# Performance work log

Measured on AMD Instinct MI355X. Metric: run time of the kernel, lower is better.

## Reference

```python
import jax, jax.numpy as jnp
import numpy as np

# Bit-slice configuration from the module defaults: slices [1,1,2,4] -> 8-bit signed INT.
# The crossbar engine's MapReduceDot decomposes the quantized integers into bit-planes,
# runs partial dot products per (input-slice, weight-slice) pair across paral_size
# partitions, and recombines them with 2^shift weights. In the ideal (noise-free)
# engine this recombination is EXACT, so the forward math equals:
#   dequant(blockwise_quant(x)) @ dequant(blockwise_quant(W^T)) + bias
# with per-block scales determined by the quant granularities.
IN_BITS = 1 + 1 + 2 + 4   # sum(input_slice)  = 8
W_BITS = 1 + 1 + 2 + 4    # sum(weight_slice) = 8
IN_GRAN = (1, 32)         # (rows, cols) blocks over (seq, in_features)
W_GRAN = (32, 32)         # blocks over (in_features, out_features) of weight.t()


def block_fake_quant(x, bits, gran):
    """Symmetric per-block fake quantization (quantize -> dequantize).

    x: [..., R, C]; gran=(gr, gc) tiles the last two dims. Each (gr, gc) block
    gets its own max-abs scale, matching SlicedData's quant_gran semantics.
    """
    qmax = float(2 ** (bits - 1) - 1)  # 127 for 8-bit
    gr, gc = gran
    lead = x.shape[:-2]
    R, C = x.shape[-2], x.shape[-1]
    xb = x.reshape(*lead, R // gr, gr, C // gc, gc)
    mx = jnp.max(jnp.abs(xb), axis=(-3, -1), keepdims=True)
    scale = jnp.where(mx > 0, mx / qmax, jnp.ones_like(mx))
    q = jnp.clip(jnp.round(xb / scale), -qmax, qmax) * scale
    return q.reshape(x.shape)


def setup_inputs() -> dict:
    key = jax.random.key(0)
    k1, k2, k3 = jax.random.split(key, 3)
    B, S, Din, Dout = 4, 4096, 2048, 2048
    x = jax.random.normal(k1, (B, S, Din), dtype=jnp.float32)
    # kaiming_uniform_(a=sqrt(5)) on a Linear weight is U(-1/sqrt(fan_in), 1/sqrt(fan_in))
    bound = 1.0 / np.sqrt(Din)
    weight = jax.random.uniform(k2, (Dout, Din), jnp.float32, -bound, bound)
    bias = jax.random.uniform(k3, (Dout,), jnp.float32, -bound, bound)
    return {"x": x, "weight": weight, "bias": bias}


def reference(x, weight, bias):
    # Quantize activations per (1, 32) block and weight.t() per (32, 32) block,
    # then recombine via the (mathematically exact) bit-sliced dot == dense GEMM
    # on the dequantized values.
    qx = block_fake_quant(x, IN_BITS, IN_GRAN)            # [B, S, Din]
    qw = block_fake_quant(weight.T, W_BITS, W_GRAN)       # [Din, Dout]
    out = jnp.einsum('bsd,de->bse', qx, qw) + bias        # [B, S, Dout]
    return out
```

## Files before the change

### kernel.cpp

```cpp
#include <hip/hip_runtime.h>
#include <hip/hip_bf16.h>
#include <stdint.h>

#define M_TOT 16384
#define N_TOT 2048
#define K_TOT 2048
#define NT 32

typedef __attribute__((ext_vector_type(8))) short bf16x8;
typedef __attribute__((ext_vector_type(4))) float f32x4;

__device__ __forceinline__ ushort f32_to_bf16_rne(float f) {
    uint32_t u = __float_as_uint(f);
    uint32_t r = (u + 0x7fffu + ((u >> 16) & 1u)) >> 16;
    return (ushort)r;
}

__device__ __forceinline__ void async_copy16(const void* gptr, void* lptr) {
    __builtin_amdgcn_global_load_lds(
        (const __attribute__((address_space(1))) uint32_t*)gptr,
        (__attribute__((address_space(3))) uint32_t*)lptr,
        16, 0, 0);
}

__global__ void quant_x_kernel(const float* __restrict__ x, ushort* __restrict__ qx) {
    const int tid = blockIdx.x * 256 + threadIdx.x;
    const float4 v = ((const float4*)x)[tid];
    float m = fmaxf(fmaxf(fabsf(v.x), fabsf(v.y)), fmaxf(fabsf(v.z), fabsf(v.w)));
    m = fmaxf(m, __shfl_xor(m, 1));
    m = fmaxf(m, __shfl_xor(m, 2));
    m = fmaxf(m, __shfl_xor(m, 4));
    const float s = (m > 0.f) ? (m / 127.f) : 1.f;
    const float q0 = fminf(fmaxf(rintf(v.x / s), -127.f), 127.f) * s;
    const float q1 = fminf(fmaxf(rintf(v.y / s), -127.f), 127.f) * s;
    const float q2 = fminf(fmaxf(rintf(v.z / s), -127.f), 127.f) * s;
    const float q3 = fminf(fmaxf(rintf(v.w / s), -127.f), 127.f) * s;
    ushort4 r;
    r.x = f32_to_bf16_rne(q0);
    r.y = f32_to_bf16_rne(q1);
    r.z = f32_to_bf16_rne(q2);
    r.w = f32_to_bf16_rne(q3);
    ((ushort4*)qx)[tid] = r;
}

__global__ void quant_w_kernel(const float* __restrict__ w, ushort* __restrict__ qw) {
    const int gtid = blockIdx.x * 256 + threadIdx.x;
    const int wid  = gtid >> 6;
    const int lane = gtid & 63;
    const int tn = wid >> 6;
    const int tk = wid & 63;
    const int row = tn * 32 + (lane >> 1);
    const int col = tk * 32 + ((lane & 1) << 4);
    const float* p = w + (size_t)row * K_TOT + col;
    const float4 v0 = ((const float4*)p)[0];
    const float4 v1 = ((const float4*)p)[1];
    const float4 v2 = ((const float4*)p)[2];
    const float4 v3 = ((const float4*)p)[3];
    float m = 0.f;
#define MAX4(V) m = fmaxf(m, fmaxf(fmaxf(fabsf(V.x), fabsf(V.y)), fmaxf(fabsf(V.z), fabsf(V.w))));
    MAX4(v0) MAX4(v1) MAX4(v2) MAX4(v3)
#undef MAX4
    #pragma unroll
    for (int off = 1; off < 64; off <<= 1) m = fmaxf(m, __shfl_xor(m, off));
    const float s = (m > 0.f) ? (m / 127.f) : 1.f;
    float vv[16] = {v0.x, v0.y, v0.z, v0.w, v1.x, v1.y, v1.z, v1.w,
                    v2.x, v2.y, v2.z, v2.w, v3.x, v3.y, v3.z, v3.w};
    union { ushort us[16]; uint4 q[2]; } o;
    #pragma unroll
    for (int i = 0; i < 16; ++i) {
        const float q = fminf(fmaxf(rintf(vv[i] / s), -127.f), 127.f) * s;
        o.us[i] = f32_to_bf16_rne(q);
    }
    uint4* dst = (uint4*)(qw + (size_t)row * K_TOT + col);
    dst[0] = o.q[0];
    dst[1] = o.q[1];
}

#define LDSA(tb, row, colus) \
    (*(const bf16x8*)&As[tb][row][(colus) ^ (((row) & 7) << 3)])
#define LDSB(tb, row, colus) \
    (*(const bf16x8*)&Bs[tb][row][(colus) ^ (((row) & 7) << 3)])

#define STAGE_A(tb, hh, li, tt)                                                          \
    async_copy16(Agbase + (size_t)((hh) * 128 + (li) * 64) * K_TOT + (size_t)(tt) * 64,  \
                 (char*)&As[0][0][0] + (tb) * 32768 + (hh) * 16384 + (li) * 8192 + (wv << 10));
#define STAGE_B(tb, hh, li, tt)                                                          \
    async_copy16(Bgbase + (size_t)((hh) * 128 + (li) * 64) * K_TOT + (size_t)(tt) * 64,  \
                 (char*)&Bs[0][0][0] + (tb) * 32768 + (hh) * 16384 + (li) * 8192 + (wv << 10));
#define STAGE_A2(tb, hh, tt)  { STAGE_A(tb, hh, 0, tt) STAGE_A(tb, hh, 1, tt) }
#define STAGE_B2(tb, hh, tt)  { STAGE_B(tb, hh, 0, tt) STAGE_B(tb, hh, 1, tt) }

#define WAITLGKM4 { asm volatile("s_waitcnt lgkmcnt(4)" ::: "memory"); __builtin_amdgcn_sched_barrier(0); }
#define WAITLGKM0 { asm volatile("s_waitcnt lgkmcnt(0)" ::: "memory"); __builtin_amdgcn_sched_barrier(0); }
#define WAITVM4   { asm volatile("s_waitcnt vmcnt(4)" ::: "memory"); }
#define WAITVM0   { asm volatile("s_waitcnt vmcnt(0)" ::: "memory"); }

#define RD_AF(DST, tb, q) {                                   \
    DST[0] = LDSA(tb, ab + (q) * 32,      h8);                \
    DST[1] = LDSA(tb, ab + (q) * 32,      32 + h8);           \
    DST[2] = LDSA(tb, ab + (q) * 32 + 16, h8);                \
    DST[3] = LDSA(tb, ab + (q) * 32 + 16, 32 + h8); }

#define MFMA_PH(i0, AF)                                                                   \
    __builtin_amdgcn_s_setprio(1);                                                        \
    _Pragma("unroll")                                                                     \
    for (int j = 0; j < 4; ++j) {                                                         \
        acc[i0][j]     = __builtin_amdgcn_mfma_f32_16x16x32_bf16(AF[0], bg[j][0], acc[i0][j], 0, 0, 0);     \
        acc[i0][j]     = __builtin_amdgcn_mfma_f32_16x16x32_bf16(AF[1], bg[j][1], acc[i0][j], 0, 0, 0);     \
        acc[(i0)+1][j] = __builtin_amdgcn_mfma_f32_16x16x32_bf16(AF[2], bg[j][0], acc[(i0)+1][j], 0, 0, 0); \
        acc[(i0)+1][j] = __builtin_amdgcn_mfma_f32_16x16x32_bf16(AF[3], bg[j][1], acc[(i0)+1][j], 0, 0, 0); \
    }                                                                                     \
    __builtin_amdgcn_s_setprio(0);

#define TILE_BODY(tb, t, STA, STB, VMC)                                                   \
  {                                                                                       \
               \
    RD_AF(afX, tb, 0)                                                                     \
    _Pragma("unroll")                                                                     \
    for (int j = 0; j < 4; ++j) {                                                         \
        const int bb = wcn * 64 + j * 16 + r;                                             \
        bg[j][0] = LDSB(tb, bb, h8);  bg[j][1] = LDSB(tb, bb, 32 + h8);                   \
    }                                                                                     \
    RD_AF(afY, tb, 1)                                                                     \
    if (STA) STAGE_A2(tb ^ 1, 0, (t) + 1)                                                 \
    WAITLGKM4                                                                             \
    MFMA_PH(0, afX)                                                                       \
                                 \
    RD_AF(afX, tb, 2)                                                                     \
    if (STA) STAGE_A2(tb ^ 1, 1, (t) + 1)                                                 \
    WAITLGKM4                                                                             \
    MFMA_PH(2, afY)                                                                       \
    __builtin_amdgcn_s_barrier();                \
                                 \
    RD_AF(afY, tb, 3)                                                                     \
    if (STB) STAGE_B2(tb, 0, (t) + 2)                                                     \
    WAITLGKM4                                                                             \
    MFMA_PH(4, afX)                                                                       \
                       \
    if (STB) STAGE_B2(tb, 1, (t) + 2)                                                     \
    WAITLGKM0                                                                             \
    MFMA_PH(6, afY)                                                                       \
    if ((VMC) == 4)      WAITVM4                                                          \
    else if ((VMC) == 0) WAITVM0                                                          \
    __builtin_amdgcn_s_barrier();                       \
  }

__global__ __launch_bounds__(512, 2) void gemm_pipe2_kernel(
    const ushort* __restrict__ A,
    const ushort* __restrict__ Bt,
    const float* __restrict__ bias,
    float* __restrict__ C) {

    __shared__ ushort As[2][256][64];
    __shared__ ushort Bs[2][256][64];

    const int tid  = threadIdx.x;
    const int lane = tid & 63;
    const int wv   = tid >> 6;
    const int wmr  = wv >> 2;
    const int wcn  = wv & 3;
    const int r    = lane & 15;
    const int h8   = (lane >> 4) << 3;

    const int nbn  = N_TOT / 256;
    const int nwg  = (M_TOT / 256) * nbn;
    const int cpx  = nwg >> 3;
    const int swz  = (blockIdx.x & 7) * cpx + (blockIdx.x >> 3);
    const int brow = (swz / nbn) * 256;
    const int bcol = (swz % nbn) * 256;

    const int srow = tid >> 3;
    const int scol = (((tid & 7) ^ (srow & 7)) << 3);
    const ushort* Agbase = A  + (size_t)(brow + srow) * K_TOT + scol;
    const ushort* Bgbase = Bt + (size_t)(bcol + srow) * K_TOT + scol;

    const int ab = wmr * 128 + r;

    f32x4 acc[8][4];
    const f32x4 zero = {0.f, 0.f, 0.f, 0.f};
    #pragma unroll
    for (int i = 0; i < 8; ++i)
        #pragma unroll
        for (int j = 0; j < 4; ++j) acc[i][j] = zero;

    STAGE_A2(0, 0, 0) STAGE_A2(0, 1, 0)
    STAGE_B2(0, 0, 0) STAGE_B2(0, 1, 0)
    STAGE_B2(1, 0, 1) STAGE_B2(1, 1, 1)
    WAITVM0
    __builtin_amdgcn_s_barrier();

    bf16x8 afX[4], afY[4];
    bf16x8 bg[4][2];

    for (int t = 0; t < NT - 2; t += 2) {
        TILE_BODY(0, t,     1, 1, 4)
        TILE_BODY(1, t + 1, 1, 1, 4)
    }
    TILE_BODY(0, NT - 2, 1, 0, 0)
    TILE_BODY(1, NT - 1, 0, 0, -1)

    const int hq = (lane >> 4) * 4;
    float bv[4];
    #pragma unroll
    for (int j = 0; j < 4; ++j) bv[j] = bias[bcol + wcn * 64 + j * 16 + r];
    #pragma unroll
    for (int i = 0; i < 8; ++i) {
        const int row0 = brow + wmr * 128 + i * 16 + hq;
        #pragma unroll
        for (int j = 0; j < 4; ++j) {
            const int col = bcol + wcn * 64 + j * 16 + r;
            #pragma unroll
            for (int jj = 0; jj < 4; ++jj)
                C[(size_t)(row0 + jj) * N_TOT + col] = acc[i][j][jj] + bv[j];
        }
    }
}

extern "C" void kernel_launch(void* const* d_in, const int* in_sizes, int n_in,
                              void* d_out, int out_size, void* d_ws, size_t ws_size,
                              hipStream_t stream) {
    const float* x    = (const float*)d_in[0];
    const float* wgt  = (const float*)d_in[1];
    const float* bias = (const float*)d_in[2];
    float* out = (float*)d_out;

    ushort* qx = (ushort*)d_ws;
    ushort* qw = qx + (size_t)M_TOT * K_TOT;

    quant_x_kernel<<<(M_TOT * K_TOT / 4) / 256, 256, 0, stream>>>(x, qx);
    quant_w_kernel<<<(64 * 64 * 64) / 256, 256, 0, stream>>>(wgt, qw);
    gemm_pipe2_kernel<<<(M_TOT / 256) * (N_TOT / 256), 512, 0, stream>>>(qx, qw, bias, out);
}
```

Measured before the change: 166.3 us.

## Prefetch next tile's B fragments and split vmcnt waits across phases

Moves the LDS reads of B fragments for the next K-tile to the end of the current tile body, so they overlap the tail MFMA phase instead of stalling the next tile's start. The vmcnt wait for the A half is moved to mid-tile, with a barrier, before the second MFMA phase. The B wait stays at the end, so the initial wait only covers the first tile. This reshuffles the cross-stage schedule and synchronisation to hide LDS latency. It adds register pressure and risks ordering hazards on the double-buffered LDS.

```diff
diff --git a/kernel.cpp b/kernel.cpp
--- a/kernel.cpp
+++ b/kernel.cpp
@@ -92,14 +92,19 @@
 
 #define WAITLGKM4 { asm volatile("s_waitcnt lgkmcnt(4)" ::: "memory"); __builtin_amdgcn_sched_barrier(0); }
 #define WAITLGKM0 { asm volatile("s_waitcnt lgkmcnt(0)" ::: "memory"); __builtin_amdgcn_sched_barrier(0); }
-#define WAITVM4   { asm volatile("s_waitcnt vmcnt(4)" ::: "memory"); }
-#define WAITVM0   { asm volatile("s_waitcnt vmcnt(0)" ::: "memory"); }
 
 #define RD_AF(DST, tb, q) {                                   \
     DST[0] = LDSA(tb, ab + (q) * 32,      h8);                \
     DST[1] = LDSA(tb, ab + (q) * 32,      32 + h8);           \
     DST[2] = LDSA(tb, ab + (q) * 32 + 16, h8);                \
     DST[3] = LDSA(tb, ab + (q) * 32 + 16, 32 + h8); }
+
+#define RD_BG(tb) {                                                           \
+    _Pragma("unroll")                                                         \
+    for (int j = 0; j < 4; ++j) {                                             \
+        const int bb = wcn * 64 + j * 16 + r;                                 \
+        bg[j][0] = LDSB(tb, bb, h8);  bg[j][1] = LDSB(tb, bb, 32 + h8);       \
+    } }
 
 #define MFMA_PH(i0, AF)                                                                   \
     __builtin_amdgcn_s_setprio(1);                                                        \
@@ -112,40 +117,39 @@
     }                                                                                     \
     __builtin_amdgcn_s_setprio(0);
 
-#define TILE_BODY(tb, t, STA, STB, VMC)                                                   \
+#define TILE_BODY(tb, t, STA, STB, RDBG, VM1, VM3)                                        \
   {                                                                                       \
-               \
+                                                                            \
     RD_AF(afX, tb, 0)                                                                     \
-    _Pragma("unroll")                                                                     \
-    for (int j = 0; j < 4; ++j) {                                                         \
-        const int bb = wcn * 64 + j * 16 + r;                                             \
-        bg[j][0] = LDSB(tb, bb, h8);  bg[j][1] = LDSB(tb, bb, 32 + h8);                   \
-    }                                                                                     \
+    __builtin_amdgcn_sched_barrier(0);                                                    \
     RD_AF(afY, tb, 1)                                                                     \
     if (STA) STAGE_A2(tb ^ 1, 0, (t) + 1)                                                 \
     WAITLGKM4                                                                             \
     MFMA_PH(0, afX)                                                                       \
-                                 \
+                                                                            \
     RD_AF(afX, tb, 2)                                                                     \
     if (STA) STAGE_A2(tb ^ 1, 1, (t) + 1)                                                 \
+    if ((VM1) == 4) { asm volatile("s_waitcnt vmcnt(4)" ::: "memory"); }                  \
+    else if ((VM1) == 0) { asm volatile("s_waitcnt vmcnt(0)" ::: "memory"); }             \
+    __builtin_amdgcn_s_barrier();           \
     WAITLGKM4                                                                             \
     MFMA_PH(2, afY)                                                                       \
-    __builtin_amdgcn_s_barrier();                \
-                                 \
+                                                                            \
     RD_AF(afY, tb, 3)                                                                     \
     if (STB) STAGE_B2(tb, 0, (t) + 2)                                                     \
     WAITLGKM4                                                                             \
     MFMA_PH(4, afX)                                                                       \
-                       \
+                                                                            \
     if (STB) STAGE_B2(tb, 1, (t) + 2)                                                     \
     WAITLGKM0                                                                             \
     MFMA_PH(6, afY)                                                                       \
-    if ((VMC) == 4)      WAITVM4                                                          \
-    else if ((VMC) == 0) WAITVM0                                                          \
-    __builtin_amdgcn_s_barrier();                       \
+    if (RDBG) RD_BG((tb) ^ 1)      \
+    if ((VM3) == 4) { asm volatile("s_waitcnt vmcnt(4)" ::: "memory"); }                  \
+    else if ((VM3) == 0) { asm volatile("s_waitcnt vmcnt(0)" ::: "memory"); }             \
+    __builtin_amdgcn_s_barrier();                         \
   }
 
-__global__ __launch_bounds__(512, 2) void gemm_pipe2_kernel(
+__global__ __launch_bounds__(512, 2) void gemm_pipe3_kernel(
     const ushort* __restrict__ A,
     const ushort* __restrict__ Bt,
     const float* __restrict__ bias,
@@ -186,18 +190,20 @@
     STAGE_A2(0, 0, 0) STAGE_A2(0, 1, 0)
     STAGE_B2(0, 0, 0) STAGE_B2(0, 1, 0)
     STAGE_B2(1, 0, 1) STAGE_B2(1, 1, 1)
-    WAITVM0
+    asm volatile("s_waitcnt vmcnt(4)" ::: "memory");
     __builtin_amdgcn_s_barrier();
 
     bf16x8 afX[4], afY[4];
     bf16x8 bg[4][2];
+    RD_BG(0)
+    __builtin_amdgcn_sched_barrier(0);
 
     for (int t = 0; t < NT - 2; t += 2) {
-        TILE_BODY(0, t,     1, 1, 4)
-        TILE_BODY(1, t + 1, 1, 1, 4)
+        TILE_BODY(0, t,     1, 1, 1, 4, 4)
+        TILE_BODY(1, t + 1, 1, 1, 1, 4, 4)
     }
-    TILE_BODY(0, NT - 2, 1, 0, 0)
-    TILE_BODY(1, NT - 1, 0, 0, -1)
+    TILE_BODY(0, NT - 2, 1, 0, 1, 4, 0)
+    TILE_BODY(1, NT - 1, 0, 0, 0, -1, -1)
 
     const int hq = (lane >> 4) * 4;
     float bv[4];
@@ -229,5 +235,5 @@
 
     quant_x_kernel<<<(M_TOT * K_TOT / 4) / 256, 256, 0, stream>>>(x, qx);
     quant_w_kernel<<<(64 * 64 * 64) / 256, 256, 0, stream>>>(wgt, qw);
-    gemm_pipe2_kernel<<<(M_TOT / 256) * (N_TOT / 256), 512, 0, stream>>>(qx, qw, bias, out);
-}
+    gemm_pipe3_kernel<<<(M_TOT / 256) * (N_TOT / 256), 512, 0, stream>>>(qx, qw, bias, out);
+}
```

Result: no change. 169.2 us (+1.8%).
